# Kernel optimization log

Measured on AMD Instinct MI355X. Metric: run time of the kernel, lower is better.

The kernel has to match this reference:

```python
import jax, jax.numpy as jnp
import numpy as np

BATCH = 128
SPEC_STEPS = 8
VOCAB = 128000


def setup_inputs() -> dict:
    key = jax.random.key(0)
    k1, k2, k3 = jax.random.split(key, 3)
    # Ragged draft counts per request in [1, SPEC_STEPS]
    counts = np.random.default_rng(0).integers(1, SPEC_STEPS + 1, size=BATCH)
    cu = np.cumsum(counts).astype(np.int32)
    num_tokens = int(cu[-1])
    draft_token_ids = jax.random.randint(k1, (num_tokens,), 0, VOCAB, dtype=jnp.int32)
    target_logits = jax.random.normal(k2, (num_tokens, VOCAB), dtype=jnp.float32)
    bonus_token_ids = jax.random.randint(k3, (BATCH,), 0, VOCAB, dtype=jnp.int32)
    return {
        "draft_token_ids": draft_token_ids,
        "num_spec_steps": SPEC_STEPS,
        "cu_num_draft_tokens": jnp.asarray(cu),
        "target_logits": target_logits,
        "bonus_token_ids": bonus_token_ids,
    }


def reference(draft_token_ids, num_spec_steps, cu_num_draft_tokens, target_logits, bonus_token_ids):
    INVALID = jnp.int32(-1)
    S = num_spec_steps  # python int
    # Greedy target token per draft position: [T]
    target_argmax = jnp.argmax(target_logits, axis=-1).astype(jnp.int32)

    starts = jnp.concatenate([jnp.zeros((1,), cu_num_draft_tokens.dtype), cu_num_draft_tokens[:-1]])
    n_draft = (cu_num_draft_tokens - starts).astype(jnp.int32)  # [B]

    pos = jnp.arange(S, dtype=jnp.int32)                 # [S]
    valid = pos[None, :] < n_draft[:, None]              # [B,S] pos < num_draft
    tok_idx = jnp.where(valid, starts[:, None].astype(jnp.int32) + pos[None, :], 0)
    d = draft_token_ids[tok_idx]                         # [B,S]
    t = target_argmax[tok_idx]                           # [B,S]

    mismatch = valid & (d != t)                          # [B,S]
    mi = mismatch.astype(jnp.int32)
    # rejected BEFORE this position (kernel stores argmax at the mismatch pos itself)
    prev_rejected = (jnp.cumsum(mi, axis=1) - mi) > 0    # exclusive prefix any-mismatch
    written = jnp.where(prev_rejected, INVALID, t)       # value stored at pos < num_draft

    rejected = jnp.any(mismatch, axis=1)                 # [B]
    processed = jnp.sum((valid & ~prev_rejected).astype(jnp.int32), axis=1)
    num_bonus_tokens = (processed - 1 + (~rejected).astype(jnp.int32)).astype(jnp.int32)

    bonus_col = jnp.where(rejected, INVALID, bonus_token_ids)  # [B]

    pos2 = jnp.arange(S + 1, dtype=jnp.int32)[None, :]   # [1,S+1]
    written_p = jnp.pad(written, ((0, 0), (0, 1)), constant_values=-1)
    output_token_ids = jnp.where(
        pos2 < n_draft[:, None], written_p,
        jnp.where(pos2 == n_draft[:, None], bonus_col[:, None], INVALID)
    ).astype(jnp.int32)  # [B, S+1]; slots past bonus are -1 (torch version leaves them uninitialized)

    return output_token_ids, num_bonus_tokens
```

## Files before the change

kernel.cpp:

```cpp
#include <hip/hip_runtime.h>
#include <hip/hip_bf16.h>
#include <math.h>


__device__ __forceinline__ void combine(float& bv, int& bi, float v, int i) {
    if (v > bv || (v == bv && i < bi)) { bv = v; bi = i; }
}

template <int BLOCK>
__global__ void __launch_bounds__(BLOCK)
argmax_rows_kernel(const float* __restrict__ logits, int vocab,
                   int* __restrict__ out_idx) {
    const int row = blockIdx.x;
    const float* rowp = logits + (size_t)row * (size_t)vocab;
    const int tid = threadIdx.x;

    float bv = -INFINITY;
    int   bi = 0x7fffffff;

    const int nv4 = vocab >> 2;
    const float4* p4 = (const float4*)rowp;
    for (int j = tid; j < nv4; j += BLOCK) {
        float4 v = p4[j];
        const int base = j << 2;
        combine(bv, bi, v.x, base + 0);
        combine(bv, bi, v.y, base + 1);
        combine(bv, bi, v.z, base + 2);
        combine(bv, bi, v.w, base + 3);
    }
    for (int j = (nv4 << 2) + tid; j < vocab; j += BLOCK) {
        combine(bv, bi, rowp[j], j);
    }

    #pragma unroll
    for (int off = 32; off >= 1; off >>= 1) {
        float ov = __shfl_down(bv, off, 64);
        int   oi = __shfl_down(bi, off, 64);
        combine(bv, bi, ov, oi);
    }

    constexpr int NW = BLOCK / 64;
    __shared__ float sv[NW];
    __shared__ int   si[NW];
    const int wave = tid >> 6;
    if ((tid & 63) == 0) { sv[wave] = bv; si[wave] = bi; }
    __syncthreads();
    if (tid == 0) {
        #pragma unroll
        for (int w = 1; w < NW; ++w) combine(bv, bi, sv[w], si[w]);
        out_idx[row] = bi;
    }
}

__global__ void finalize_kernel(const int* __restrict__ draft,
                                const int* __restrict__ cu,
                                const int* __restrict__ argmax_idx,
                                const int* __restrict__ bonus,
                                int* __restrict__ out_tokens,
                                int* __restrict__ out_bonus,
                                int B, int S) {
    const int b = blockIdx.x * blockDim.x + threadIdx.x;
    if (b >= B) return;
    const int start = (b == 0) ? 0 : cu[b - 1];
    const int n     = cu[b] - start;
    int* row = out_tokens + (size_t)b * (S + 1);

    bool rejected  = false;
    int  processed = 0;
    for (int p = 0; p < S + 1; ++p) {
        int val;
        if (p < n) {
            if (!rejected) {
                const int t = argmax_idx[start + p];
                val = t;
                ++processed;
                if (draft[start + p] != t) rejected = true;
            } else {
                val = -1;
            }
        } else if (p == n) {
            val = rejected ? -1 : bonus[b];
        } else {
            val = -1;
        }
        row[p] = val;
    }
    out_bonus[b] = processed - 1 + (rejected ? 0 : 1);
}

extern "C" void kernel_launch(void* const* d_in, const int* in_sizes, int n_in,
                              void* d_out, int out_size, void* d_ws, size_t ws_size,
                              hipStream_t stream) {
    const int*   draft  = (const int*)d_in[0];
    const int*   cu     = (const int*)d_in[2];
    const float* logits = (const float*)d_in[3];
    const int*   bonus  = (const int*)d_in[4];

    const int T     = in_sizes[0];
    const int B     = in_sizes[2];
    const int vocab = in_sizes[3] / T;
    const int S     = out_size / B - 2;

    int* argmax_buf = (int*)d_ws;
    int* out_tokens = (int*)d_out;
    int* out_bonus  = out_tokens + (size_t)B * (S + 1);

    constexpr int BLOCK = 512;
    argmax_rows_kernel<BLOCK><<<T, BLOCK, 0, stream>>>(logits, vocab, argmax_buf);
    finalize_kernel<<<(B + 127) / 128, 128, 0, stream>>>(
        draft, cu, argmax_buf, bonus, out_tokens, out_bonus, B, S);
}
```

Before: 65.42 us.

## Split each row's argmax across 8 blocks and merge partials in finalize

The row argmax is split into 8 vocabulary segments, each handled by its own 256-thread block that writes a partial (value, index) pair to workspace. The finalize kernel then merges the 8 partials per token before comparing against the draft. Loads switch to nontemporal vector loads. The aim is more blocks in flight and more memory parallelism across the ~580 rows. The cost is extra workspace traffic and a serial merge in the finalize step.

```diff
diff --git a/kernel.cpp b/kernel.cpp
--- a/kernel.cpp
+++ b/kernel.cpp
@@ -3,32 +3,41 @@
 #include <math.h>
 
 
+typedef float f32x4 __attribute__((ext_vector_type(4)));
+
 __device__ __forceinline__ void combine(float& bv, int& bi, float v, int i) {
     if (v > bv || (v == bv && i < bi)) { bv = v; bi = i; }
 }
 
-template <int BLOCK>
+template <int BLOCK, int NS>
 __global__ void __launch_bounds__(BLOCK)
-argmax_rows_kernel(const float* __restrict__ logits, int vocab,
-                   int* __restrict__ out_idx) {
-    const int row = blockIdx.x;
+argmax_partial_kernel(const float* __restrict__ logits, int vocab,
+                      float* __restrict__ ws_val, int* __restrict__ ws_idx) {
+    const int bid = blockIdx.x;
+    const int row = bid / NS;
+    const int seg = bid % NS;
+    const int seg_len = vocab / NS;
+    const int seg_beg = seg * seg_len;
+    const int seg_end = (seg == NS - 1) ? vocab : seg_beg + seg_len;
+
     const float* rowp = logits + (size_t)row * (size_t)vocab;
     const int tid = threadIdx.x;
 
     float bv = -INFINITY;
     int   bi = 0x7fffffff;
 
-    const int nv4 = vocab >> 2;
-    const float4* p4 = (const float4*)rowp;
-    for (int j = tid; j < nv4; j += BLOCK) {
-        float4 v = p4[j];
+    const int beg4 = seg_beg >> 2;
+    const int end4 = seg_end >> 2;
+    const f32x4* p4 = (const f32x4*)rowp;
+    for (int j = beg4 + tid; j < end4; j += BLOCK) {
+        f32x4 v = __builtin_nontemporal_load(&p4[j]);
         const int base = j << 2;
         combine(bv, bi, v.x, base + 0);
         combine(bv, bi, v.y, base + 1);
         combine(bv, bi, v.z, base + 2);
         combine(bv, bi, v.w, base + 3);
     }
-    for (int j = (nv4 << 2) + tid; j < vocab; j += BLOCK) {
+    for (int j = (end4 << 2) + tid; j < seg_end; j += BLOCK) {
         combine(bv, bi, rowp[j], j);
     }
 
@@ -48,13 +57,16 @@
     if (tid == 0) {
         #pragma unroll
         for (int w = 1; w < NW; ++w) combine(bv, bi, sv[w], si[w]);
-        out_idx[row] = bi;
+        ws_val[bid] = bv;
+        ws_idx[bid] = bi;
     }
 }
 
+template <int NS>
 __global__ void finalize_kernel(const int* __restrict__ draft,
                                 const int* __restrict__ cu,
-                                const int* __restrict__ argmax_idx,
+                                const float* __restrict__ ws_val,
+                                const int* __restrict__ ws_idx,
                                 const int* __restrict__ bonus,
                                 int* __restrict__ out_tokens,
                                 int* __restrict__ out_bonus,
@@ -71,10 +83,15 @@
         int val;
         if (p < n) {
             if (!rejected) {
-                const int t = argmax_idx[start + p];
-                val = t;
+                const int base = (start + p) * NS;
+                float bv = -INFINITY;
+                int   bi = 0x7fffffff;
+                #pragma unroll
+                for (int s = 0; s < NS; ++s)
+                    combine(bv, bi, ws_val[base + s], ws_idx[base + s]);
+                val = bi;
                 ++processed;
-                if (draft[start + p] != t) rejected = true;
+                if (draft[start + p] != bi) rejected = true;
             } else {
                 val = -1;
             }
@@ -101,12 +118,16 @@
     const int vocab = in_sizes[3] / T;
     const int S     = out_size / B - 2;
 
-    int* argmax_buf = (int*)d_ws;
+    constexpr int NS    = 8;
+    constexpr int BLOCK = 256;
+
+    float* ws_val = (float*)d_ws;
+    int*   ws_idx = (int*)(ws_val + (size_t)T * NS);
     int* out_tokens = (int*)d_out;
     int* out_bonus  = out_tokens + (size_t)B * (S + 1);
 
-    constexpr int BLOCK = 512;
-    argmax_rows_kernel<BLOCK><<<T, BLOCK, 0, stream>>>(logits, vocab, argmax_buf);
-    finalize_kernel<<<(B + 127) / 128, 128, 0, stream>>>(
-        draft, cu, argmax_buf, bonus, out_tokens, out_bonus, B, S);
+    argmax_partial_kernel<BLOCK, NS><<<T * NS, BLOCK, 0, stream>>>(
+        logits, vocab, ws_val, ws_idx);
+    finalize_kernel<NS><<<(B + 127) / 128, 128, 0, stream>>>(
+        draft, cu, ws_val, ws_idx, bonus, out_tokens, out_bonus, B, S);
 }
```

Result: faster. 59.21 us (-9.5%).

## Split argmax rows into per-wave chunks with two-stage reduction in finalize

Applied to the files above, without the earlier changes.

Replaces the one-block-per-row argmax with many independent wavefronts, each scanning a fixed 5120-element chunk using unrolled nontemporal vector loads and four independent running maxima. Per-chunk partial results go to workspace and are merged per token inside a rewritten finalize kernel. This targets more memory-level parallelism and removes the block-wide LDS reduction and barrier for a bandwidth-bound scan. The cost is extra workspace traffic and a serial merge of 25 partials per token in finalize, plus reliance on the strict '>' per-lane tie order to keep first-index semantics.

```diff
diff --git a/kernel.cpp b/kernel.cpp
--- a/kernel.cpp
+++ b/kernel.cpp
@@ -3,34 +3,80 @@
 #include <math.h>
 
 
+typedef float f32x4 __attribute__((ext_vector_type(4)));
+
+constexpr int U_F4        = 20;
+constexpr int CHUNK_ELEMS = 64 * 4 * U_F4;
+
 __device__ __forceinline__ void combine(float& bv, int& bi, float v, int i) {
     if (v > bv || (v == bv && i < bi)) { bv = v; bi = i; }
 }
 
-template <int BLOCK>
+template <int BLOCK, bool EXACT>
 __global__ void __launch_bounds__(BLOCK)
-argmax_rows_kernel(const float* __restrict__ logits, int vocab,
-                   int* __restrict__ out_idx) {
-    const int row = blockIdx.x;
-    const float* rowp = logits + (size_t)row * (size_t)vocab;
-    const int tid = threadIdx.x;
+argmax_wave_chunks(const float* __restrict__ logits, int vocab,
+                   int chunks_per_row, int nwaves,
+                   float* __restrict__ ws_val, int* __restrict__ ws_idx) {
+    const int wid = blockIdx.x * (BLOCK / 64) + (threadIdx.x >> 6);
+    if (wid >= nwaves) return;
+    const int lane = threadIdx.x & 63;
+    const int row  = wid / chunks_per_row;
+    const int ch   = wid - row * chunks_per_row;
+    const int chunk_beg = ch * CHUNK_ELEMS;
+    const float* base = logits + (size_t)row * (size_t)vocab + chunk_beg;
+    const f32x4* p4 = (const f32x4*)base;
 
-    float bv = -INFINITY;
-    int   bi = 0x7fffffff;
+    float bv0 = -INFINITY, bv1 = -INFINITY, bv2 = -INFINITY, bv3 = -INFINITY;
+    int   bj0 = 0, bj1 = 1, bj2 = 2, bj3 = 3;
 
-    const int nv4 = vocab >> 2;
-    const float4* p4 = (const float4*)rowp;
-    for (int j = tid; j < nv4; j += BLOCK) {
-        float4 v = p4[j];
-        const int base = j << 2;
-        combine(bv, bi, v.x, base + 0);
-        combine(bv, bi, v.y, base + 1);
-        combine(bv, bi, v.z, base + 2);
-        combine(bv, bi, v.w, base + 3);
+    if (EXACT) {
+        #pragma unroll
+        for (int g = 0; g < U_F4; g += 4) {
+            const f32x4 a = __builtin_nontemporal_load(p4 + (g + 0) * 64 + lane);
+            const f32x4 b = __builtin_nontemporal_load(p4 + (g + 1) * 64 + lane);
+            const f32x4 c = __builtin_nontemporal_load(p4 + (g + 2) * 64 + lane);
+            const f32x4 d = __builtin_nontemporal_load(p4 + (g + 3) * 64 + lane);
+            const int ea = ((g + 0) * 64 + lane) << 2;
+            const int eb = ((g + 1) * 64 + lane) << 2;
+            const int ec = ((g + 2) * 64 + lane) << 2;
+            const int ed = ((g + 3) * 64 + lane) << 2;
+            if (a.x > bv0) { bv0 = a.x; bj0 = ea; }
+            if (a.y > bv1) { bv1 = a.y; bj1 = ea + 1; }
+            if (a.z > bv2) { bv2 = a.z; bj2 = ea + 2; }
+            if (a.w > bv3) { bv3 = a.w; bj3 = ea + 3; }
+            if (b.x > bv0) { bv0 = b.x; bj0 = eb; }
+            if (b.y > bv1) { bv1 = b.y; bj1 = eb + 1; }
+            if (b.z > bv2) { bv2 = b.z; bj2 = eb + 2; }
+            if (b.w > bv3) { bv3 = b.w; bj3 = eb + 3; }
+            if (c.x > bv0) { bv0 = c.x; bj0 = ec; }
+            if (c.y > bv1) { bv1 = c.y; bj1 = ec + 1; }
+            if (c.z > bv2) { bv2 = c.z; bj2 = ec + 2; }
+            if (c.w > bv3) { bv3 = c.w; bj3 = ec + 3; }
+            if (d.x > bv0) { bv0 = d.x; bj0 = ed; }
+            if (d.y > bv1) { bv1 = d.y; bj1 = ed + 1; }
+            if (d.z > bv2) { bv2 = d.z; bj2 = ed + 2; }
+            if (d.w > bv3) { bv3 = d.w; bj3 = ed + 3; }
+        }
+    } else {
+        const int chunk_len = min(CHUNK_ELEMS, vocab - chunk_beg);
+        const int n4 = chunk_len >> 2;
+        for (int s = lane; s < n4; s += 64) {
+            const f32x4 a = __builtin_nontemporal_load(p4 + s);
+            const int e = s << 2;
+            if (a.x > bv0) { bv0 = a.x; bj0 = e; }
+            if (a.y > bv1) { bv1 = a.y; bj1 = e + 1; }
+            if (a.z > bv2) { bv2 = a.z; bj2 = e + 2; }
+            if (a.w > bv3) { bv3 = a.w; bj3 = e + 3; }
+        }
+        for (int e = (n4 << 2) + lane; e < chunk_len; e += 64)
+            combine(bv0, bj0, base[e], e);
     }
-    for (int j = (nv4 << 2) + tid; j < vocab; j += BLOCK) {
-        combine(bv, bi, rowp[j], j);
-    }
+
+    float bv = bv0; int bi = bj0;
+    combine(bv, bi, bv1, bj1);
+    combine(bv, bi, bv2, bj2);
+    combine(bv, bi, bv3, bj3);
+    bi += chunk_beg;
 
     #pragma unroll
     for (int off = 32; off >= 1; off >>= 1) {
@@ -38,54 +84,57 @@
         int   oi = __shfl_down(bi, off, 64);
         combine(bv, bi, ov, oi);
     }
-
-    constexpr int NW = BLOCK / 64;
-    __shared__ float sv[NW];
-    __shared__ int   si[NW];
-    const int wave = tid >> 6;
-    if ((tid & 63) == 0) { sv[wave] = bv; si[wave] = bi; }
-    __syncthreads();
-    if (tid == 0) {
-        #pragma unroll
-        for (int w = 1; w < NW; ++w) combine(bv, bi, sv[w], si[w]);
-        out_idx[row] = bi;
-    }
+    if (lane == 0) { ws_val[wid] = bv; ws_idx[wid] = bi; }
 }
 
-__global__ void finalize_kernel(const int* __restrict__ draft,
-                                const int* __restrict__ cu,
-                                const int* __restrict__ argmax_idx,
-                                const int* __restrict__ bonus,
-                                int* __restrict__ out_tokens,
-                                int* __restrict__ out_bonus,
-                                int B, int S) {
-    const int b = blockIdx.x * blockDim.x + threadIdx.x;
-    if (b >= B) return;
+__global__ void __launch_bounds__(64)
+finalize_kernel(const int* __restrict__ draft,
+                const int* __restrict__ cu,
+                const float* __restrict__ ws_val,
+                const int* __restrict__ ws_idx,
+                const int* __restrict__ bonus,
+                int* __restrict__ out_tokens,
+                int* __restrict__ out_bonus,
+                int chunks_per_row, int S) {
+    const int b = blockIdx.x;
+    const int lane = threadIdx.x;
     const int start = (b == 0) ? 0 : cu[b - 1];
-    const int n     = cu[b] - start;
-    int* row = out_tokens + (size_t)b * (S + 1);
+    const int n = cu[b] - start;
 
-    bool rejected  = false;
-    int  processed = 0;
-    for (int p = 0; p < S + 1; ++p) {
-        int val;
-        if (p < n) {
-            if (!rejected) {
-                const int t = argmax_idx[start + p];
-                val = t;
-                ++processed;
-                if (draft[start + p] != t) rejected = true;
+    __shared__ int tok[32];
+    if (lane < n && lane < 32) {
+        const int base = (start + lane) * chunks_per_row;
+        float bv = -INFINITY;
+        int   bi = 0x7fffffff;
+        for (int k = 0; k < chunks_per_row; ++k)
+            combine(bv, bi, ws_val[base + k], ws_idx[base + k]);
+        tok[lane] = bi;
+    }
+    __syncthreads();
+    if (lane == 0) {
+        int* rowo = out_tokens + (size_t)b * (S + 1);
+        bool rejected  = false;
+        int  processed = 0;
+        for (int p = 0; p <= S; ++p) {
+            int val;
+            if (p < n) {
+                if (!rejected) {
+                    const int t = tok[p];
+                    val = t;
+                    ++processed;
+                    if (draft[start + p] != t) rejected = true;
+                } else {
+                    val = -1;
+                }
+            } else if (p == n) {
+                val = rejected ? -1 : bonus[b];
             } else {
                 val = -1;
             }
-        } else if (p == n) {
-            val = rejected ? -1 : bonus[b];
-        } else {
-            val = -1;
+            rowo[p] = val;
         }
-        row[p] = val;
+        out_bonus[b] = processed - 1 + (rejected ? 0 : 1);
     }
-    out_bonus[b] = processed - 1 + (rejected ? 0 : 1);
 }
 
 extern "C" void kernel_launch(void* const* d_in, const int* in_sizes, int n_in,
@@ -101,12 +150,24 @@
     const int vocab = in_sizes[3] / T;
     const int S     = out_size / B - 2;
 
-    int* argmax_buf = (int*)d_ws;
+    constexpr int BLOCK = 256;
+    const bool exact = (vocab % CHUNK_ELEMS) == 0;
+    const int cpr    = (vocab + CHUNK_ELEMS - 1) / CHUNK_ELEMS;
+    const int nwaves = T * cpr;
+    const int blocks = (nwaves + (BLOCK / 64) - 1) / (BLOCK / 64);
+
+    float* ws_val = (float*)d_ws;
+    int*   ws_idx = (int*)(ws_val + (size_t)T * cpr);
     int* out_tokens = (int*)d_out;
     int* out_bonus  = out_tokens + (size_t)B * (S + 1);
 
-    constexpr int BLOCK = 512;
-    argmax_rows_kernel<BLOCK><<<T, BLOCK, 0, stream>>>(logits, vocab, argmax_buf);
-    finalize_kernel<<<(B + 127) / 128, 128, 0, stream>>>(
-        draft, cu, argmax_buf, bonus, out_tokens, out_bonus, B, S);
+    if (exact) {
+        argmax_wave_chunks<BLOCK, true><<<blocks, BLOCK, 0, stream>>>(
+            logits, vocab, cpr, nwaves, ws_val, ws_idx);
+    } else {
+        argmax_wave_chunks<BLOCK, false><<<blocks, BLOCK, 0, stream>>>(
+            logits, vocab, cpr, nwaves, ws_val, ws_idx);
+    }
+    finalize_kernel<<<B, 64, 0, stream>>>(
+        draft, cu, ws_val, ws_idx, bonus, out_tokens, out_bonus, cpr, S);
 }
```

After: 54.15 us, median of 2. 17.2% less time.
